# Kernel optimization log

Hardware: AMD Instinct MI355X
Metric: run time of the kernel (lower is better)

The kernel has to match this reference:

```python
import jax, jax.numpy as jnp
import numpy as np

N, E = 100000, 1600000
IN_C, HID, NUM_CLASSES = 128, 256, 15
EPS = 1e-5


def setup_inputs() -> dict:
    key = jax.random.key(0)
    ks = jax.random.split(key, 20)

    def lin(k, out_c, in_c):
        # torch Linear default init: U(-1/sqrt(in), 1/sqrt(in))
        bound = 1.0 / np.sqrt(in_c)
        return jax.random.uniform(k, (out_c, in_c), jnp.float32, -bound, bound)

    inp = {
        'x': jax.random.normal(ks[0], (N, IN_C), jnp.float32),
        'edge_index': jax.random.randint(ks[1], (2, E), 0, N, jnp.int64),
        # conv1: SAGEConv(IN_C -> HID): lin_l (with bias) on aggregated msgs, lin_r (no bias) on root
        'w1_l': lin(ks[2], HID, IN_C), 'b1_l': jnp.zeros((HID,), jnp.float32), 'w1_r': lin(ks[3], HID, IN_C),
        'g1': jnp.ones((HID,), jnp.float32), 'be1': jnp.zeros((HID,), jnp.float32),
        # conv2: HID -> HID
        'w2_l': lin(ks[4], HID, HID), 'b2_l': jnp.zeros((HID,), jnp.float32), 'w2_r': lin(ks[5], HID, HID),
        'g2': jnp.ones((HID,), jnp.float32), 'be2': jnp.zeros((HID,), jnp.float32),
        # conv3: HID -> HID//2
        'w3_l': lin(ks[6], HID // 2, HID), 'b3_l': jnp.zeros((HID // 2,), jnp.float32), 'w3_r': lin(ks[7], HID // 2, HID),
        'g3': jnp.ones((HID // 2,), jnp.float32), 'be3': jnp.zeros((HID // 2,), jnp.float32),
        # classifier
        'wc': lin(ks[8], NUM_CLASSES, HID // 2), 'bc': jnp.zeros((NUM_CLASSES,), jnp.float32),
    }
    return inp


def _sage(x, src, dst, w_l, b_l, w_r):
    # PyG SAGEConv (aggr='mean'): lin_l(mean_{j in N(i)} x_j) + lin_r(x_i)
    n = x.shape[0]
    agg = jax.ops.segment_sum(x[src], dst, num_segments=n)            # [N, d]
    deg = jax.ops.segment_sum(jnp.ones_like(dst, dtype=x.dtype), dst, num_segments=n)
    mean = agg / jnp.maximum(deg, 1.0)[:, None]
    return mean @ w_l.T + b_l + x @ w_r.T


def _bn_relu(x, g, b):
    # BatchNorm1d in training mode: biased batch stats over node dim, then ReLU
    mu = jnp.mean(x, axis=0)
    var = jnp.mean((x - mu) ** 2, axis=0)
    return jax.nn.relu((x - mu) * jax.lax.rsqrt(var + EPS) * g + b)


def reference(x, edge_index, w1_l, b1_l, w1_r, g1, be1, w2_l, b2_l, w2_r, g2, be2,
              w3_l, b3_l, w3_r, g3, be3, wc, bc):
    src, dst = edge_index[0], edge_index[1]
    h = _bn_relu(_sage(x, src, dst, w1_l, b1_l, w1_r), g1, be1)   # dropout = identity (eval)
    h = _bn_relu(_sage(h, src, dst, w2_l, b2_l, w2_r), g2, be2)
    h = _bn_relu(_sage(h, src, dst, w3_l, b3_l, w3_r), g3, be3)
    return h @ wc.T + bc
```

## Files before the change

kernel.cpp:

```cpp
#include <hip/hip_runtime.h>


#define DEV static __device__ __forceinline__

typedef unsigned short us;
typedef __attribute__((ext_vector_type(8))) __bf16 bf16x8;
typedef __attribute__((ext_vector_type(4))) float f32x4;

DEV float bf2f(us u) { return __uint_as_float(((unsigned)u) << 16); }
DEV us f2bf(float f) {
    unsigned u = __float_as_uint(f);
    unsigned r = u + 0x7fffu + ((u >> 16) & 1u);
    return (us)(r >> 16);
}

typedef __attribute__((address_space(3))) void lds_void;
typedef const __attribute__((address_space(1))) void gbl_void;
DEV void gll16(const void* g, void* l) {
    __builtin_amdgcn_global_load_lds((gbl_void*)g, (lds_void*)l, 16, 0, 0);
}

DEV bool is_i64(const int* ei) {
    return (ei[1] == 0) & (ei[3] == 0) & (ei[5] == 0) & (ei[7] == 0);
}

DEV void rowacc2(float* acc, unsigned u) {
    acc[0] += __uint_as_float(u << 16);
    acc[1] += __uint_as_float(u & 0xffff0000u);
}
DEV void rowacc4(float* acc, uint2 u) {
    acc[0] += __uint_as_float(u.x << 16);
    acc[1] += __uint_as_float(u.x & 0xffff0000u);
    acc[2] += __uint_as_float(u.y << 16);
    acc[3] += __uint_as_float(u.y & 0xffff0000u);
}


struct WSeg { const float* s; us* d; int n4; int l2w4; int stride; };
struct WConvAll { WSeg seg[8]; };


__global__ void prep0(WConvAll wc, const int* __restrict__ ei, int E,
                      int* __restrict__ hist2, int NB, int chunk) {
    __shared__ int h[256];
    const int t = threadIdx.x;
    if (blockIdx.x < 256) {
        const int g = blockIdx.x;
        const bool i64 = is_i64(ei);
        h[t] = 0;
        __syncthreads();
        int beg = g * chunk, end = min(beg + chunk, E);
        for (int e = beg + t; e < end; e += 256) {
            int d = i64 ? ei[2 * (E + e)] : ei[E + e];
            atomicAdd(&h[d >> 9], 1);
        }
        __syncthreads();
        if (t < NB) hist2[g * NB + t] = h[t];
    } else {
        const int bid = blockIdx.x - 256;
        for (int sg = 0; sg < 8; ++sg) {
            WSeg w = wc.seg[sg];
            for (int i = bid * 256 + t; i < w.n4; i += 1024 * 256) {
                float4 v = ((const float4*)w.s)[i];
                ushort4 r;
                r.x = f2bf(v.x); r.y = f2bf(v.y); r.z = f2bf(v.z); r.w = f2bf(v.w);
                int row = i >> w.l2w4;
                int col = (i - (row << w.l2w4)) * 4;
                *(ushort4*)(w.d + (size_t)row * w.stride + col) = r;
            }
        }
    }
}


__global__ void bucket_offsets(int* __restrict__ hist2, int* __restrict__ bucketBase,
                               int* __restrict__ rp, int N, int G, int NB) {
    __shared__ int tot[256];
    const int t = threadIdx.x;
    int sum = 0;
    if (t < NB)
        for (int g = 0; g < G; ++g) sum += hist2[g * NB + t];
    tot[t] = sum;
    __syncthreads();
    for (int off = 1; off < 256; off <<= 1) {
        int v = (t >= off) ? tot[t - off] : 0;
        __syncthreads();
        tot[t] += v;
        __syncthreads();
    }
    int base = tot[t] - sum;
    if (t < NB) {
        bucketBase[t] = base;
        int run = base;
        for (int g = 0; g < G; ++g) {
            int v = hist2[g * NB + t];
            hist2[g * NB + t] = run;
            run += v;
        }
        if (t == NB - 1) {
            bucketBase[NB] = tot[t];
            rp[N] = tot[t];
        }
    }
}

__global__ void scatter8(const int* __restrict__ ei, int E, const int* __restrict__ hist2,
                         uint2* __restrict__ ebuf, int NB, int chunk) {
    __shared__ int off[256];
    const int g = blockIdx.x, t = threadIdx.x;
    const bool i64 = is_i64(ei);
    if (t < NB) off[t] = hist2[g * NB + t];
    __syncthreads();
    int beg = g * chunk, end = min(beg + chunk, E);
    for (int e = beg + t; e < end; e += 256) {
        int s = i64 ? ei[2 * e] : ei[e];
        int d = i64 ? ei[2 * (E + e)] : ei[E + e];
        int p = atomicAdd(&off[d >> 9], 1);
        ebuf[p] = make_uint2((unsigned)s, (unsigned)d);
    }
}

__global__ void fine_csr(const uint2* __restrict__ ebuf, const int* __restrict__ bucketBase,
                         int N, int* __restrict__ rp, int* __restrict__ csr) {
    __shared__ int cnt[512];
    __shared__ int red[256];
    const int b = blockIdx.x, t = threadIdx.x;
    const int node0 = b << 9;
    cnt[t] = 0;
    cnt[t + 256] = 0;
    __syncthreads();
    const int ebeg = bucketBase[b], eend = bucketBase[b + 1];
    for (int e = ebeg + t; e < eend; e += 256) {
        uint2 r = ebuf[e];
        atomicAdd(&cnt[r.y & 511], 1);
    }
    __syncthreads();
    int c0 = cnt[2 * t], c1 = cnt[2 * t + 1];
    int s = c0 + c1;
    red[t] = s;
    __syncthreads();
    for (int off = 1; off < 256; off <<= 1) {
        int v = (t >= off) ? red[t - off] : 0;
        __syncthreads();
        red[t] += v;
        __syncthreads();
    }
    int pre = red[t] - s;
    int n0 = node0 + 2 * t;
    if (n0 < N) rp[n0] = ebeg + pre;
    if (n0 + 1 < N) rp[n0 + 1] = ebeg + pre + c0;
    __syncthreads();
    cnt[2 * t] = ebeg + pre;
    cnt[2 * t + 1] = ebeg + pre + c0;
    __syncthreads();
    for (int e = ebeg + t; e < eend; e += 256) {
        uint2 r = ebuf[e];
        int p = atomicAdd(&cnt[r.y & 511], 1);
        csr[p] = (int)r.x;
    }
}


template <int VEC>
__global__ void agg_mean(const us* __restrict__ X, const int* __restrict__ rp,
                         const int* __restrict__ csr, us* __restrict__ M, int n) {
    const int cols = VEC * 64;
    int w = blockIdx.x * (blockDim.x >> 6) + (threadIdx.x >> 6);
    int lane = threadIdx.x & 63;
    if (w >= n) return;
    int beg = rp[w], end = rp[w + 1];
    const us* Xb = X + lane * VEC;
    float acc[VEC];
#pragma unroll
    for (int i = 0; i < VEC; ++i) acc[i] = 0.f;
    int e = beg;
    int cnt = end - beg;
    if (VEC == 2) {
        if (cnt >= 8) {
            int j[4];
            unsigned u[4], un[4];
#pragma unroll
            for (int q = 0; q < 4; ++q) j[q] = csr[e + q];
#pragma unroll
            for (int q = 0; q < 4; ++q) u[q] = *(const unsigned*)(Xb + (size_t)j[q] * cols);
            for (e = beg + 4; e + 4 <= end; e += 4) {
#pragma unroll
                for (int q = 0; q < 4; ++q) j[q] = csr[e + q];
#pragma unroll
                for (int q = 0; q < 4; ++q) un[q] = *(const unsigned*)(Xb + (size_t)j[q] * cols);
#pragma unroll
                for (int q = 0; q < 4; ++q) rowacc2(acc, u[q]);
#pragma unroll
                for (int q = 0; q < 4; ++q) u[q] = un[q];
            }
#pragma unroll
            for (int q = 0; q < 4; ++q) rowacc2(acc, u[q]);
        }
        for (; e < end; ++e) rowacc2(acc, *(const unsigned*)(Xb + (size_t)csr[e] * cols));
    } else {
        if (cnt >= 8) {
            int j[4];
            uint2 u[4], un[4];
#pragma unroll
            for (int q = 0; q < 4; ++q) j[q] = csr[e + q];
#pragma unroll
            for (int q = 0; q < 4; ++q) u[q] = *(const uint2*)(Xb + (size_t)j[q] * cols);
            for (e = beg + 4; e + 4 <= end; e += 4) {
#pragma unroll
                for (int q = 0; q < 4; ++q) j[q] = csr[e + q];
#pragma unroll
                for (int q = 0; q < 4; ++q) un[q] = *(const uint2*)(Xb + (size_t)j[q] * cols);
#pragma unroll
                for (int q = 0; q < 4; ++q) rowacc4(acc, u[q]);
#pragma unroll
                for (int q = 0; q < 4; ++q) u[q] = un[q];
            }
#pragma unroll
            for (int q = 0; q < 4; ++q) rowacc4(acc, u[q]);
        }
        for (; e < end; ++e) rowacc4(acc, *(const uint2*)(Xb + (size_t)csr[e] * cols));
    }
    float inv = 1.0f / (float)max(cnt, 1);
    us* q = M + (size_t)w * cols + lane * VEC;
    if (VEC == 2) {
        *(ushort2*)q = make_ushort2(f2bf(acc[0] * inv), f2bf(acc[1] * inv));
    } else {
        *(ushort4*)q = make_ushort4(f2bf(acc[0] * inv), f2bf(acc[1] * inv),
                                    f2bf(acc[2] * inv), f2bf(acc[3] * inv));
    }
}

__global__ void agg_post(const us* __restrict__ Yc, const int* __restrict__ rp,
                         const int* __restrict__ csr, const float* __restrict__ bias,
                         us* __restrict__ H, int n) {
    int w = blockIdx.x * (blockDim.x >> 6) + (threadIdx.x >> 6);
    int lane = threadIdx.x & 63;
    if (w >= n) return;
    int beg = rp[w], end = rp[w + 1];
    const us* Yb = Yc + lane * 2;
    float acc[2] = {0.f, 0.f};
    int e = beg;
    int cnt = end - beg;
    if (cnt >= 8) {
        int j[4];
        unsigned u[4], un[4];
#pragma unroll
        for (int q = 0; q < 4; ++q) j[q] = csr[e + q];
#pragma unroll
        for (int q = 0; q < 4; ++q) u[q] = *(const unsigned*)(Yb + (size_t)j[q] * 256);
        for (e = beg + 4; e + 4 <= end; e += 4) {
#pragma unroll
            for (int q = 0; q < 4; ++q) j[q] = csr[e + q];
#pragma unroll
            for (int q = 0; q < 4; ++q) un[q] = *(const unsigned*)(Yb + (size_t)j[q] * 256);
#pragma unroll
            for (int q = 0; q < 4; ++q) rowacc2(acc, u[q]);
#pragma unroll
            for (int q = 0; q < 4; ++q) u[q] = un[q];
        }
#pragma unroll
        for (int q = 0; q < 4; ++q) rowacc2(acc, u[q]);
    }
    for (; e < end; ++e) rowacc2(acc, *(const unsigned*)(Yb + (size_t)csr[e] * 256));
    float inv = 1.0f / (float)max(cnt, 1);
    unsigned uz = *(const unsigned*)(Yc + (size_t)w * 256 + 128 + lane * 2);
    float2 bv = *(const float2*)(bias + lane * 2);
    float r0 = acc[0] * inv + __uint_as_float(uz << 16) + bv.x;
    float r1 = acc[1] * inv + __uint_as_float(uz & 0xffff0000u) + bv.y;
    *(ushort2*)(H + (size_t)w * 128 + lane * 2) = make_ushort2(f2bf(r0), f2bf(r1));
}


template <int THREADS, int BM, int BN, int WM, int WN>
__launch_bounds__(THREADS)
__global__ void gemm_mfma(const us* __restrict__ A0, int K0,
                          const us* __restrict__ A1, int K1,
                          const us* __restrict__ W, const float* __restrict__ bias,
                          int n, int outc, us* __restrict__ Cbf, float* __restrict__ Cf,
                          float* __restrict__ st0, float* __restrict__ st1) {
    constexpr int MT = WM / 16;
    constexpr int NT = WN / 16;
    constexpr int WCols = BN / WN;
    constexpr int NDMA = (BM * 4 + BN * 4) / THREADS;
    static_assert((BM * 4) % THREADS == 0 && (BN * 4) % THREADS == 0, "uniform DMA");
    static_assert((BM / WM) * (BN / WN) == THREADS / 64, "wave tiling");
    __shared__ __align__(16) us As[2][BM * 32];
    __shared__ __align__(16) us Bs[2][BN * 32];
    __shared__ float colred[2][BN];

    const int t = threadIdx.x;
    const int wid = t >> 6, lane = t & 63;
    const int wr = wid / WCols, wcc = wid % WCols;
    const int row0 = blockIdx.x * BM;
    const int col0 = blockIdx.y * BN;
    const int Kp = K0 + K1;
    const int nk = Kp >> 5;
    const int l15 = lane & 15, l4 = lane >> 4;

    auto issue = [&](int kidx, int p) {
        int kc = kidx << 5;
        const us* A = (kc < K0) ? A0 : A1;
        int rs = (kc < K0) ? K0 : K1;
        int ko = (kc < K0) ? kc : kc - K0;
#pragma unroll
        for (int c = t; c < BM * 4; c += THREADS) {
            int blk = c >> 6;
            int row = row0 + (blk << 4) + l15;
            gll16(A + (size_t)row * rs + ko + (l4 << 3), (char*)As[p] + blk * 1024 + lane * 16);
        }
#pragma unroll
        for (int c = t; c < BN * 4; c += THREADS) {
            int blk = c >> 6;
            int col = col0 + (blk << 4) + l15;
            gll16(W + (size_t)col * Kp + kc + (l4 << 3), (char*)Bs[p] + blk * 1024 + lane * 16);
        }
    };

    f32x4 acc[MT][NT];
#pragma unroll
    for (int i = 0; i < MT; ++i)
#pragma unroll
        for (int j = 0; j < NT; ++j) acc[i][j] = (f32x4){0.f, 0.f, 0.f, 0.f};

    issue(0, 0);
    if (nk > 1) issue(1, 1);
    for (int k = 0; k < nk; ++k) {
        if (k + 1 < nk) asm volatile("s_waitcnt vmcnt(%0)" :: "i"(NDMA) : "memory");
        else            asm volatile("s_waitcnt vmcnt(0)" ::: "memory");
        asm volatile("s_barrier" ::: "memory");
        const int p = k & 1;
        bf16x8 af[MT], bfr[NT];
#pragma unroll
        for (int mt = 0; mt < MT; ++mt)
            af[mt] = *(const bf16x8*)((char*)As[p] + (wr * MT + mt) * 1024 + lane * 16);
#pragma unroll
        for (int nt = 0; nt < NT; ++nt)
            bfr[nt] = *(const bf16x8*)((char*)Bs[p] + (wcc * NT + nt) * 1024 + lane * 16);
#pragma unroll
        for (int mt = 0; mt < MT; ++mt)
#pragma unroll
            for (int nt = 0; nt < NT; ++nt)
                acc[mt][nt] = __builtin_amdgcn_mfma_f32_16x16x32_bf16(af[mt], bfr[nt], acc[mt][nt], 0, 0, 0);
        if (k + 2 < nk) {
            asm volatile("s_barrier" ::: "memory");
            issue(k + 2, p);
        }
    }

    if (st0) {
#pragma unroll
        for (int c = t; c < 2 * BN; c += THREADS) (&colred[0][0])[c] = 0.f;
        __syncthreads();
    }

#pragma unroll
    for (int nt = 0; nt < NT; ++nt) {
        int col = col0 + wcc * WN + nt * 16 + l15;
        bool cok = col < outc;
        float bv = (bias != nullptr && cok) ? bias[col] : 0.f;
        float ls = 0.f, lq = 0.f;
#pragma unroll
        for (int mt = 0; mt < MT; ++mt) {
            int rbase = row0 + wr * WM + mt * 16 + (l4 << 2);
#pragma unroll
            for (int i = 0; i < 4; ++i) {
                int r = rbase + i;
                if (r < n && cok) {
                    float v = acc[mt][nt][i] + bv;
                    if (Cf) Cf[(size_t)r * outc + col] = v;
                    else Cbf[(size_t)r * outc + col] = f2bf(v);
                    ls += v;
                    lq += v * v;
                }
            }
        }
        if (st0 && cok) {
            int lc = wcc * WN + nt * 16 + l15;
            atomicAdd(&colred[0][lc], ls);
            atomicAdd(&colred[1][lc], lq);
        }
    }
    if (st0) {
        __syncthreads();
        int rep = (blockIdx.x & 7) << 8;
        for (int c = t; c < BN; c += THREADS) {
            if (col0 + c < outc) {
                atomicAdd(&st0[rep + col0 + c], colred[0][c]);
                atomicAdd(&st1[rep + col0 + c], colred[1][c]);
            }
        }
    }
}


__global__ void bn_stats(const us* __restrict__ H, int n, int c,
                         float* __restrict__ s0, float* __restrict__ s1) {
    int col = threadIdx.x;
    if (col >= c) return;
    float s = 0.f, q = 0.f;
    for (int r = blockIdx.x; r < n; r += gridDim.x) {
        float v = bf2f(H[(size_t)r * c + col]);
        s += v;
        q += v * v;
    }
    int rep = (blockIdx.x & 7) << 8;
    atomicAdd(&s0[rep + col], s);
    atomicAdd(&s1[rep + col], q);
}

__global__ void bn_apply(us* __restrict__ H, int n8, int c,
                         const float* __restrict__ s0, const float* __restrict__ s1,
                         const float* __restrict__ g, const float* __restrict__ be, float fn,
                         int reps, int rstride) {
    __shared__ float sc[256], sh[256];
    int t = threadIdx.x;
    if (t < c) {
        float s = 0.f, q = 0.f;
        for (int r = 0; r < reps; ++r) {
            s += s0[r * rstride + t];
            q += s1[r * rstride + t];
        }
        float mean = s / fn;
        float var = q / fn - mean * mean;
        float scale = g[t] * rsqrtf(var + 1e-5f);
        sc[t] = scale;
        sh[t] = be[t] - mean * scale;
    }
    __syncthreads();
    int cdiv8 = c >> 3;
    for (int i = blockIdx.x * blockDim.x + t; i < n8; i += gridDim.x * blockDim.x) {
        int col = (i % cdiv8) << 3;
        uint4 v = ((const uint4*)H)[i];
        float f[8];
        f[0] = __uint_as_float(v.x << 16); f[1] = __uint_as_float(v.x & 0xffff0000u);
        f[2] = __uint_as_float(v.y << 16); f[3] = __uint_as_float(v.y & 0xffff0000u);
        f[4] = __uint_as_float(v.z << 16); f[5] = __uint_as_float(v.z & 0xffff0000u);
        f[6] = __uint_as_float(v.w << 16); f[7] = __uint_as_float(v.w & 0xffff0000u);
        float4 sc0 = *(const float4*)&sc[col];
        float4 sc1 = *(const float4*)&sc[col + 4];
        float4 sh0 = *(const float4*)&sh[col];
        float4 sh1 = *(const float4*)&sh[col + 4];
        f[0] = fmaxf(f[0] * sc0.x + sh0.x, 0.f);
        f[1] = fmaxf(f[1] * sc0.y + sh0.y, 0.f);
        f[2] = fmaxf(f[2] * sc0.z + sh0.z, 0.f);
        f[3] = fmaxf(f[3] * sc0.w + sh0.w, 0.f);
        f[4] = fmaxf(f[4] * sc1.x + sh1.x, 0.f);
        f[5] = fmaxf(f[5] * sc1.y + sh1.y, 0.f);
        f[6] = fmaxf(f[6] * sc1.z + sh1.z, 0.f);
        f[7] = fmaxf(f[7] * sc1.w + sh1.w, 0.f);
        uint4 o;
        o.x = (unsigned)f2bf(f[0]) | ((unsigned)f2bf(f[1]) << 16);
        o.y = (unsigned)f2bf(f[2]) | ((unsigned)f2bf(f[3]) << 16);
        o.z = (unsigned)f2bf(f[4]) | ((unsigned)f2bf(f[5]) << 16);
        o.w = (unsigned)f2bf(f[6]) | ((unsigned)f2bf(f[7]) << 16);
        ((uint4*)H)[i] = o;
    }
}


extern "C" void kernel_launch(void* const* d_in, const int* in_sizes, int n_in,
                              void* d_out, int out_size, void* d_ws, size_t ws_size,
                              hipStream_t stream) {
    const float* x = (const float*)d_in[0];
    const int* ei = (const int*)d_in[1];
    const float* w1_l = (const float*)d_in[2];
    const float* b1_l = (const float*)d_in[3];
    const float* w1_r = (const float*)d_in[4];
    const float* g1 = (const float*)d_in[5];
    const float* be1 = (const float*)d_in[6];
    const float* w2_l = (const float*)d_in[7];
    const float* b2_l = (const float*)d_in[8];
    const float* w2_r = (const float*)d_in[9];
    const float* g2 = (const float*)d_in[10];
    const float* be2 = (const float*)d_in[11];
    const float* w3_l = (const float*)d_in[12];
    const float* b3_l = (const float*)d_in[13];
    const float* w3_r = (const float*)d_in[14];
    const float* g3 = (const float*)d_in[15];
    const float* be3 = (const float*)d_in[16];
    const float* wcf = (const float*)d_in[17];
    const float* bc = (const float*)d_in[18];

    const int N = in_sizes[0] / 128;
    const int E = in_sizes[1] / 2;
    const int NB = (N + 511) >> 9;
    const int G = 256;
    const int chunk = (E + G - 1) / G;

    char* ws = (char*)d_ws;
    size_t off = 0;
    auto alloc = [&](size_t bytes) -> char* {
        char* p = ws + off;
        off += (bytes + 255) & ~(size_t)255;
        return p;
    };
    int* rp = (int*)alloc((size_t)(N + 1) * 4);
    int* csr = (int*)alloc((size_t)E * 4);
    int* hist2 = (int*)alloc((size_t)G * NB * 4);
    int* bucketBase = (int*)alloc((size_t)(NB + 1) * 4);
    uint2* ebuf = (uint2*)alloc((size_t)E * 8);
    us* xbf = (us*)alloc((size_t)N * 128 * 2);
    us* M = (us*)alloc((size_t)N * 256 * 2);
    us* Ha = (us*)alloc((size_t)N * 256 * 2);
    us* Hb = (us*)alloc((size_t)N * 256 * 2);
    float* stats = (float*)alloc(6 * 8 * 256 * 4);
    float* s01 = stats,          *s11 = stats + 2048;
    float* s02 = stats + 4096,   *s12 = stats + 6144;
    float* s03 = stats + 8192,   *s13 = stats + 10240;
    us* wcat1 = (us*)alloc(256 * 256 * 2);
    us* wcat2 = (us*)alloc(256 * 512 * 2);
    us* w3cat = (us*)alloc(256 * 256 * 2);
    us* wc_b = (us*)alloc(64 * 128 * 2);
    alloc(1 << 20);
    (void)ws_size; (void)n_in; (void)out_size;

    hipMemsetAsync(stats, 0, 6 * 8 * 256 * 4, stream);
    WConvAll wc;
    wc.seg[0] = {x,    xbf,         N * 128 / 4,  5, 128};
    wc.seg[1] = {w1_l, wcat1,       256 * 128 / 4, 5, 256};
    wc.seg[2] = {w1_r, wcat1 + 128, 256 * 128 / 4, 5, 256};
    wc.seg[3] = {w2_l, wcat2,       256 * 256 / 4, 6, 512};
    wc.seg[4] = {w2_r, wcat2 + 256, 256 * 256 / 4, 6, 512};
    wc.seg[5] = {w3_l, w3cat,             128 * 256 / 4, 6, 256};
    wc.seg[6] = {w3_r, w3cat + 128 * 256, 128 * 256 / 4, 6, 256};
    wc.seg[7] = {wcf,  wc_b,        15 * 128 / 4,  5, 128};
    prep0<<<1280, 256, 0, stream>>>(wc, ei, E, hist2, NB, chunk);
    bucket_offsets<<<1, 256, 0, stream>>>(hist2, bucketBase, rp, N, G, NB);
    scatter8<<<G, 256, 0, stream>>>(ei, E, hist2, ebuf, NB, chunk);
    fine_csr<<<NB, 256, 0, stream>>>(ebuf, bucketBase, N, rp, csr);

    const int aggGrid = (N + 3) / 4;
    const int rowTiles = (N + 127) / 128;

    agg_mean<2><<<aggGrid, 256, 0, stream>>>(xbf, rp, csr, M, N);
    gemm_mfma<512, 128, 256, 64, 64><<<rowTiles, 512, 0, stream>>>(
        M, 128, xbf, 128, wcat1, b1_l, N, 256, Ha, nullptr, s01, s11);
    bn_apply<<<2048, 256, 0, stream>>>(Ha, N * 256 / 8, 256, s01, s11, g1, be1, (float)N, 8, 256);

    agg_mean<4><<<aggGrid, 256, 0, stream>>>(Ha, rp, csr, M, N);
    gemm_mfma<512, 128, 256, 64, 64><<<rowTiles, 512, 0, stream>>>(
        M, 256, Ha, 256, wcat2, b2_l, N, 256, Hb, nullptr, s02, s12);
    bn_apply<<<2048, 256, 0, stream>>>(Hb, N * 256 / 8, 256, s02, s12, g2, be2, (float)N, 8, 256);

    gemm_mfma<512, 128, 256, 64, 64><<<rowTiles, 512, 0, stream>>>(
        Hb, 256, nullptr, 0, w3cat, nullptr, N, 256, M, nullptr, nullptr, nullptr);
    agg_post<<<aggGrid, 256, 0, stream>>>(M, rp, csr, b3_l, Ha, N);
    bn_stats<<<1024, 256, 0, stream>>>(Ha, N, 128, s03, s13);
    bn_apply<<<2048, 256, 0, stream>>>(Ha, N * 128 / 8, 128, s03, s13, g3, be3, (float)N, 8, 256);

    gemm_mfma<256, 128, 64, 128, 16><<<rowTiles, 256, 0, stream>>>(
        Ha, 128, nullptr, 0, wc_b, bc, N, 15, nullptr, (float*)d_out, nullptr, nullptr);
}
```

Before: 786.9 us.

## Fuse layer-1 mean aggregation into the MFMA GEMM via LDS staging

Adds a gemm_g1 kernel that gathers neighbor means for its 128-row tile directly into shared memory in MFMA fragment layout. It then runs the concatenated [mean | x] GEMM, streaming the root-feature half of the A operand from global memory. This removes the separate agg_mean launch and the write and re-read of the intermediate aggregate buffer. In exchange, each block does a serial gather phase before any MFMA work, with only one wave per row, which may lower overlap and occupancy given the large LDS footprint.

Result: slower. 921.7 us (+17.1%).

```diff
diff --git a/kernel.cpp b/kernel.cpp
--- a/kernel.cpp
+++ b/kernel.cpp
@@ -268,6 +268,164 @@
     float r0 = acc[0] * inv + __uint_as_float(uz << 16) + bv.x;
     float r1 = acc[1] * inv + __uint_as_float(uz & 0xffff0000u) + bv.y;
     *(ushort2*)(H + (size_t)w * 128 + lane * 2) = make_ushort2(f2bf(r0), f2bf(r1));
+}
+
+__launch_bounds__(512)
+__global__ void gemm_g1(const us* __restrict__ X, const int* __restrict__ rp,
+                        const int* __restrict__ csr, const us* __restrict__ W,
+                        const float* __restrict__ bias, int n,
+                        us* __restrict__ C, float* __restrict__ st0,
+                        float* __restrict__ st1) {
+    __shared__ __align__(16) us Aall[4 * 4096];
+    __shared__ __align__(16) us Bs[2][256 * 32];
+    __shared__ float colred[2][256];
+
+    const int t = threadIdx.x;
+    const int wid = t >> 6, lane = t & 63;
+    const int wr = wid >> 2, wcc = wid & 3;
+    const int row0 = blockIdx.x * 128;
+    const int l15 = lane & 15, l4 = lane >> 4;
+
+    auto issueB = [&](int kidx, int p) {
+#pragma unroll
+        for (int c = t; c < 1024; c += 512) {
+            int blk = c >> 6;
+            int col = (blk << 4) + l15;
+            gll16(W + (size_t)col * 256 + (kidx << 5) + (l4 << 3),
+                  (char*)Bs[p] + blk * 1024 + lane * 16);
+        }
+    };
+
+    issueB(0, 0);
+    issueB(1, 1);
+
+    {
+        const us* Xb = X + lane * 2;
+        const int kpart = (lane >> 4) * 4096;
+        const int usbase = wid * 512 + (((lane >> 2) & 3) << 7) + ((lane & 3) << 1);
+        for (int i = 0; i < 16; ++i) {
+            int w = row0 + (wid << 4) + i;
+            float a0 = 0.f, a1 = 0.f;
+            int cnt = 0;
+            if (w < n) {
+                int beg = rp[w], end = rp[w + 1];
+                cnt = end - beg;
+                int e = beg;
+                if (cnt >= 8) {
+                    int j[4];
+                    unsigned u[4], un[4];
+#pragma unroll
+                    for (int q = 0; q < 4; ++q) j[q] = csr[e + q];
+#pragma unroll
+                    for (int q = 0; q < 4; ++q) u[q] = *(const unsigned*)(Xb + (size_t)j[q] * 128);
+                    for (e = beg + 4; e + 4 <= end; e += 4) {
+#pragma unroll
+                        for (int q = 0; q < 4; ++q) j[q] = csr[e + q];
+#pragma unroll
+                        for (int q = 0; q < 4; ++q) un[q] = *(const unsigned*)(Xb + (size_t)j[q] * 128);
+#pragma unroll
+                        for (int q = 0; q < 4; ++q) {
+                            a0 += __uint_as_float(u[q] << 16);
+                            a1 += __uint_as_float(u[q] & 0xffff0000u);
+                        }
+#pragma unroll
+                        for (int q = 0; q < 4; ++q) u[q] = un[q];
+                    }
+#pragma unroll
+                    for (int q = 0; q < 4; ++q) {
+                        a0 += __uint_as_float(u[q] << 16);
+                        a1 += __uint_as_float(u[q] & 0xffff0000u);
+                    }
+                }
+                for (; e < end; ++e) {
+                    unsigned u0 = *(const unsigned*)(Xb + (size_t)csr[e] * 128);
+                    a0 += __uint_as_float(u0 << 16);
+                    a1 += __uint_as_float(u0 & 0xffff0000u);
+                }
+            }
+            float inv = 1.0f / (float)max(cnt, 1);
+            *(ushort2*)(Aall + kpart + usbase + i * 8) =
+                make_ushort2(f2bf(a0 * inv), f2bf(a1 * inv));
+        }
+    }
+    __syncthreads();
+
+    f32x4 acc[4][4];
+#pragma unroll
+    for (int i = 0; i < 4; ++i)
+#pragma unroll
+        for (int j = 0; j < 4; ++j) acc[i][j] = (f32x4){0.f, 0.f, 0.f, 0.f};
+
+    bf16x8 afc[4], afn[4];
+    for (int k = 0; k < 8; ++k) {
+        if (k < 7) asm volatile("s_waitcnt vmcnt(2)" ::: "memory");
+        else       asm volatile("s_waitcnt vmcnt(0)" ::: "memory");
+        asm volatile("s_barrier" ::: "memory");
+        const int p = k & 1;
+        bf16x8 bfr[4];
+#pragma unroll
+        for (int nt = 0; nt < 4; ++nt)
+            bfr[nt] = *(const bf16x8*)((char*)Bs[p] + (wcc * 4 + nt) * 1024 + lane * 16);
+        if (k < 4) {
+#pragma unroll
+            for (int mt = 0; mt < 4; ++mt)
+                afc[mt] = *(const bf16x8*)((char*)Aall + k * 8192 + (wr * 4 + mt) * 1024 + lane * 16);
+        }
+#pragma unroll
+        for (int mt = 0; mt < 4; ++mt)
+#pragma unroll
+            for (int nt = 0; nt < 4; ++nt)
+                acc[mt][nt] = __builtin_amdgcn_mfma_f32_16x16x32_bf16(afc[mt], bfr[nt], acc[mt][nt], 0, 0, 0);
+        if (k >= 3 && k < 7) {
+            int kk = k - 3;
+#pragma unroll
+            for (int mt = 0; mt < 4; ++mt)
+                afn[mt] = *(const bf16x8*)(X + (size_t)(row0 + wr * 64 + mt * 16 + l15) * 128 + kk * 32 + (l4 << 3));
+        }
+        asm volatile("s_barrier" ::: "memory");
+        if (k + 2 < 8) issueB(k + 2, p);
+        if (k >= 3) {
+#pragma unroll
+            for (int mt = 0; mt < 4; ++mt) afc[mt] = afn[mt];
+        }
+    }
+
+#pragma unroll
+    for (int c = t; c < 512; c += 512) { colred[0][c & 255] = 0.f; }
+    {
+#pragma unroll
+        for (int c = t; c < 2 * 256; c += 512) (&colred[0][0])[c] = 0.f;
+    }
+    __syncthreads();
+
+#pragma unroll
+    for (int nt = 0; nt < 4; ++nt) {
+        int col = wcc * 64 + nt * 16 + l15;
+        float bv = bias[col];
+        float ls = 0.f, lq = 0.f;
+#pragma unroll
+        for (int mt = 0; mt < 4; ++mt) {
+            int rbase = row0 + wr * 64 + mt * 16 + (l4 << 2);
+#pragma unroll
+            for (int i = 0; i < 4; ++i) {
+                int r = rbase + i;
+                if (r < n) {
+                    float v = acc[mt][nt][i] + bv;
+                    C[(size_t)r * 256 + col] = f2bf(v);
+                    ls += v;
+                    lq += v * v;
+                }
+            }
+        }
+        atomicAdd(&colred[0][col], ls);
+        atomicAdd(&colred[1][col], lq);
+    }
+    __syncthreads();
+    int rep = (blockIdx.x & 7) << 8;
+    for (int c = t; c < 256; c += 512) {
+        atomicAdd(&st0[rep + c], colred[0][c]);
+        atomicAdd(&st1[rep + c], colred[1][c]);
+    }
 }
 
 
@@ -532,9 +690,7 @@
     const int aggGrid = (N + 3) / 4;
     const int rowTiles = (N + 127) / 128;
 
-    agg_mean<2><<<aggGrid, 256, 0, stream>>>(xbf, rp, csr, M, N);
-    gemm_mfma<512, 128, 256, 64, 64><<<rowTiles, 512, 0, stream>>>(
-        M, 128, xbf, 128, wcat1, b1_l, N, 256, Ha, nullptr, s01, s11);
+    gemm_g1<<<rowTiles, 512, 0, stream>>>(xbf, rp, csr, wcat1, b1_l, N, Ha, s01, s11);
     bn_apply<<<2048, 256, 0, stream>>>(Ha, N * 256 / 8, 256, s01, s11, g1, be1, (float)N, 8, 256);
 
     agg_mean<4><<<aggGrid, 256, 0, stream>>>(Ha, rp, csr, M, N);
```
